# Optimization experiments

Hardware: AMD Instinct MI355X
Metric: run time of the kernel (lower is better)

The kernel has to match this reference:

```python
import jax, jax.numpy as jnp
import numpy as np

RADIUS = 0.1
NSAMPLE = 32


def _ball_query(new_xyz, xyz, radius, nsample):
    # new_xyz: (B, S, 3), xyz: (B, N, 3) -> idx (B, S, nsample) int32
    N = xyz.shape[1]
    d2 = jnp.sum((new_xyz[:, :, None, :] - xyz[:, None, :, :]) ** 2, axis=-1)  # (B,S,N)
    mask = d2 < radius * radius
    cand = jnp.where(mask, jnp.arange(N, dtype=jnp.int32)[None, None, :], N)
    cand = jnp.sort(cand, axis=-1)[:, :, :nsample]  # first nsample in-ball indices
    first = cand[:, :, :1]
    first = jnp.where(first == N, 0, first)  # empty ball -> index 0 (CUDA semantics)
    return jnp.where(cand == N, first, cand).astype(jnp.int32)


def _group(features, idx):
    # features: (B, C, N), idx: (B, S, K) -> (B, C, S, K)
    return jax.vmap(lambda f, i: f[:, i])(features, idx)


def setup_inputs() -> dict:
    key = jax.random.key(0)
    k1, k2, k3, k4 = jax.random.split(key, 4)
    B, N, S, C = 4, 16384, 2048, 64
    xyz = jax.random.uniform(k1, (B, N, 3), dtype=jnp.float32)
    new_xyz = jax.random.uniform(k2, (B, S, 3), dtype=jnp.float32)
    features = jax.random.normal(k3, (B, C, N), dtype=jnp.float32)
    fps_idx = jax.random.randint(k4, (B, S), 0, N, dtype=jnp.int32)
    return {"xyz": xyz, "new_xyz": new_xyz, "features": features, "fps_idx": fps_idx}


def reference(xyz, new_xyz, features, fps_idx):
    idx = _ball_query(new_xyz, xyz, RADIUS, NSAMPLE)          # (B,S,nsample)
    idx = jnp.concatenate([fps_idx[:, :, None], idx], axis=2)  # (B,S,nsample+1)
    xyz_t = jnp.transpose(xyz, (0, 2, 1))                      # (B,3,N)
    raw_grouped_xyz = _group(xyz_t, idx)                       # (B,3,S,K)
    grouped_xyz = raw_grouped_xyz - jnp.transpose(new_xyz, (0, 2, 1))[..., None]
    grouped_features = _group(features, idx)                   # (B,C,S,K)
    return jnp.concatenate([raw_grouped_xyz, grouped_xyz, grouped_features], axis=1)
```

## Files before the change

### kernel.cpp

```cpp
#include <hip/hip_runtime.h>

#define BB 4
#define NN 16384
#define SS 2048
#define CC 64
#define NS 32
#define KK 33
#define OC 70
#define SCH 4
#define GT 512
#define NC 10
#define NCELL 1000
#define CCAP 64
#define HCAP 224
#define RPAD 0.100001f

__device__ __forceinline__ float sq_nofma(float v) {
  float r = v * v;
  asm volatile("" : "+v"(r));
  return r;
}

__device__ __forceinline__ int cell1(float x) {
  int c = (int)(x * 10.0f);
  return c < 0 ? 0 : (c > 9 ? 9 : c);
}
__device__ __forceinline__ int cell3(float x, float y, float z) {
  return (cell1(z) * NC + cell1(y)) * NC + cell1(x);
}

__device__ __forceinline__ void ball_query_wave(
    const float* __restrict__ xb, float qx, float qy, float qz, int lane,
    int* out) {
  const float R2 = 0.01f;
  int cnt = 0;
  int firstIdx = 0;
  for (int base = 0; base < NN; base += 256) {
    float px[4], py[4], pz[4];
#pragma unroll
    for (int j = 0; j < 4; ++j) {
      int n = base + j * 64 + lane;
      const float* p = xb + n * 3;
      px[j] = p[0]; py[j] = p[1]; pz[j] = p[2];
    }
#pragma unroll
    for (int j = 0; j < 4; ++j) {
      float dx = px[j] - qx, dy = py[j] - qy, dz = pz[j] - qz;
      float d2 = sq_nofma(dx) + sq_nofma(dy);
      asm volatile("" : "+v"(d2));
      d2 = d2 + sq_nofma(dz);
      bool m = d2 < R2;
      unsigned long long bal = __ballot(m);
      if (cnt == 0 && bal) firstIdx = base + j * 64 + __builtin_ctzll(bal);
      int pos = cnt + (int)__popcll(bal & ((1ull << lane) - 1ull));
      if (m && pos < NS) out[pos] = base + j * 64 + lane;
      cnt += (int)__popcll(bal);
    }
    if (cnt >= NS) break;
  }
  if (cnt < NS) {
    int pad = (cnt == 0) ? 0 : firstIdx;
    if (lane >= cnt && lane < NS) out[lane] = pad;
  }
}

__global__ __launch_bounds__(256) void qg_tr_build(
    const float* __restrict__ xyz, const float* __restrict__ feat,
    float* __restrict__ featT, int* __restrict__ cnt, int* __restrict__ ovf,
    float4* __restrict__ ptsc) {
  __shared__ float tile[32 * 260];
  const int bid = (int)blockIdx.x;
  const int tid = (int)threadIdx.x;
  const int b = bid >> 7;
  const int rest = bid & 127;
  const int n0 = (rest >> 1) << 8;
  const int cc = rest & 1;
  const int c0 = cc << 5;
  const int wv = tid >> 6, lane = tid & 63;

  if (cc == 0) {
    const int n = n0 + tid;
    const float* p = xyz + ((size_t)b * NN + n) * 3;
    float x = p[0], y = p[1], z = p[2];
    int cell = cell3(x, y, z);
    int pos = atomicAdd(&cnt[(b << 10) + cell], 1);
    if (pos < CCAP) {
      ptsc[((((size_t)b << 10) + cell) << 6) + pos] =
          make_float4(x, y, z, __int_as_float(n));
    } else {
      atomicOr(&ovf[b], 1);
    }
  }

  const float* fb = feat + ((size_t)b * CC + c0) * NN + n0;
#pragma unroll
  for (int rr = 0; rr < 8; ++rr) {
    int c = rr * 4 + wv;
    float4 v = *(const float4*)(fb + (size_t)c * NN + 4 * lane);
    *(float4*)&tile[c * 260 + 4 * lane] = v;
  }
  __syncthreads();
  const int c4 = lane & 7, m = lane >> 3;
  float4* oT = (float4*)(featT + ((size_t)b * NN + n0) * CC);
#pragma unroll
  for (int it = 0; it < 8; ++it) {
    int n = it * 32 + wv * 8 + m;
    float4 v;
    v.x = tile[(4 * c4 + 0) * 260 + n];
    v.y = tile[(4 * c4 + 1) * 260 + n];
    v.z = tile[(4 * c4 + 2) * 260 + n];
    v.w = tile[(4 * c4 + 3) * 260 + n];
    oT[(size_t)n * (CC / 4) + (c0 >> 2) + c4] = v;
  }
}

__global__ __launch_bounds__(GT) void qg_main(
    const float* __restrict__ xyz, const float* __restrict__ nxyz,
    const float4* __restrict__ ptsc, const int* __restrict__ cnt,
    const int* __restrict__ ovf, const float* __restrict__ featT,
    const int* __restrict__ fps, float* __restrict__ out) {
  __shared__ float sf[CC][SCH * KK + 1];
  __shared__ int sidx[SCH * KK];
  __shared__ int hitbuf[SCH][HCAP];
  const int tid = (int)threadIdx.x;
  const int blk = (int)blockIdx.x;
  const int b = blk >> 9;
  const int s0 = (blk & 511) * SCH;
  const int wv = tid >> 6, lane = tid & 63;

  if (wv < SCH) {
    const int q = b * SS + s0 + wv;
    const float R2 = 0.01f;
    float qx = nxyz[q * 3 + 0];
    float qy = nxyz[q * 3 + 1];
    float qz = nxyz[q * 3 + 2];
    int* hb = hitbuf[wv];
    int* qout = &sidx[wv * KK];

    if (ovf[b]) {
      ball_query_wave(xyz + (size_t)b * NN * 3, qx, qy, qz, lane, qout + 1);
    } else {
      int lox = max(0, (int)floorf((qx - RPAD) * 10.f));
      int hix = min(9, (int)floorf((qx + RPAD) * 10.f));
      int loy = max(0, (int)floorf((qy - RPAD) * 10.f));
      int hiy = min(9, (int)floorf((qy + RPAD) * 10.f));
      int loz = max(0, (int)floorf((qz - RPAD) * 10.f));
      int hiz = min(9, (int)floorf((qz + RPAD) * 10.f));
      const int ncx = hix - lox + 1, ncy = hiy - loy + 1, ncz = hiz - loz + 1;
      const int ncell = ncx * ncy * ncz;

      const int* cntb = cnt + (b << 10);
      int cell_l = 0, cnt_l = 0;
      if (lane < ncell) {
        int iz = lane / (ncx * ncy);
        int r = lane - iz * ncx * ncy;
        int iy = r / ncx, ix = r - iy * ncx;
        cell_l = ((loz + iz) * NC + (loy + iy)) * NC + (lox + ix);
        cnt_l = cntb[cell_l];
      }

      const float4* pcb = ptsc + ((size_t)b << 16);
      const unsigned long long lt = (1ull << lane) - 1ull;
      const int slot = lane & 31;
      const int half = lane >> 5;
      int hcnt = 0;
      const int npair = (ncell + 1) >> 1;

      int c0 = __shfl(cell_l, 0, 64);
      int c1 = __shfl(cell_l, 1, 64);
      float4 vnext = pcb[(((half ? c1 : c0)) << 6) + slot];

      for (int p = 0; p < npair; ++p) {
        float4 v = vnext;
        int m0 = __shfl(cnt_l, 2 * p, 64);
        int m1 = __shfl(cnt_l, 2 * p + 1, 64);
        int cme0 = __shfl(cell_l, 2 * p, 64);
        int cme1 = __shfl(cell_l, 2 * p + 1, 64);
        if (p + 1 < npair) {
          int n0 = __shfl(cell_l, 2 * p + 2, 64);
          int n1 = __shfl(cell_l, 2 * p + 3, 64);
          vnext = pcb[(((half ? n1 : n0)) << 6) + slot];
        }
        int m = half ? m1 : m0;
        {
          float dx = v.x - qx, dy = v.y - qy, dz = v.z - qz;
          float d2 = sq_nofma(dx) + sq_nofma(dy);
          asm volatile("" : "+v"(d2));
          d2 = d2 + sq_nofma(dz);
          bool hit = (slot < m) && (d2 < R2);
          unsigned long long bal = __ballot(hit);
          if (hit) {
            int pos = hcnt + (int)__popcll(bal & lt);
            if (pos < HCAP) hb[pos] = __float_as_int(v.w);
          }
          hcnt += (int)__popcll(bal);
        }
        if (m0 > 32 || m1 > 32) {
          float4 w = pcb[(((half ? cme1 : cme0)) << 6) + 32 + slot];
          float dx = w.x - qx, dy = w.y - qy, dz = w.z - qz;
          float d2 = sq_nofma(dx) + sq_nofma(dy);
          asm volatile("" : "+v"(d2));
          d2 = d2 + sq_nofma(dz);
          bool hit = (32 + slot < m) && (d2 < R2);
          unsigned long long bal = __ballot(hit);
          if (hit) {
            int pos = hcnt + (int)__popcll(bal & lt);
            if (pos < HCAP) hb[pos] = __float_as_int(w.w);
          }
          hcnt += (int)__popcll(bal);
        }
      }

      asm volatile("s_waitcnt lgkmcnt(0)" ::: "memory");
      const int M = hcnt;
      if (M > HCAP) {
        ball_query_wave(xyz + (size_t)b * NN * 3, qx, qy, qz, lane, qout + 1);
      } else {
        int minv = 0x7fffffff;
        for (int i = lane; i < M; i += 64) {
          int hh = hb[i];
          minv = min(minv, hh);
          int rank = 0;
          for (int j = 0; j < M; ++j) rank += (hb[j] < hh) ? 1 : 0;
          if (rank < NS) qout[1 + rank] = hh;
        }
        if (M < NS) {
#pragma unroll
          for (int d = 1; d < 64; d <<= 1)
            minv = min(minv, __shfl_xor(minv, d, 64));
          int pad = (M == 0) ? 0 : minv;
          if (lane >= M && lane < NS) qout[1 + lane] = pad;
        }
      }
    }
    if (lane == 0) qout[0] = fps[q];
  }
  __syncthreads();

  const size_t cstr = (size_t)SS * KK;
  const float4* fT4 = (const float4*)(featT + (size_t)b * NN * CC);
  int e = tid & 15;
  for (int pp = tid >> 4; pp < SCH * KK; pp += GT / 16) {
    int n = sidx[pp];
    float4 v = fT4[(size_t)n * (CC / 4) + e];
    sf[4 * e + 0][pp] = v.x;
    sf[4 * e + 1][pp] = v.y;
    sf[4 * e + 2][pp] = v.z;
    sf[4 * e + 3][pp] = v.w;
  }

  if (tid < SCH * KK) {
    int s4 = tid / KK;
    int n = sidx[tid];
    const float* p = xyz + ((size_t)b * NN + n) * 3;
    float x = p[0], y = p[1], z = p[2];
    int q = b * SS + s0 + s4;
    float cx = nxyz[q * 3 + 0], cy = nxyz[q * 3 + 1], cz = nxyz[q * 3 + 2];
    size_t obase = ((size_t)(b * OC) * SS + s0) * KK + tid;
    out[obase + 0 * cstr] = x;
    out[obase + 1 * cstr] = y;
    out[obase + 2 * cstr] = z;
    out[obase + 3 * cstr] = x - cx;
    out[obase + 4 * cstr] = y - cy;
    out[obase + 5 * cstr] = z - cz;
  }
  __syncthreads();

  size_t fbase = ((size_t)(b * OC + 6) * SS + s0) * KK;
  for (int idx = tid; idx < CC * SCH * KK; idx += GT) {
    int c = idx / (SCH * KK);
    int j = idx - c * (SCH * KK);
    out[fbase + (size_t)c * cstr + j] = sf[c][j];
  }
}

__global__ __launch_bounds__(256) void qg_ballq(
    const float* __restrict__ xyz, const float* __restrict__ nxyz,
    int* __restrict__ wsidx) {
  int q = (int)((blockIdx.x * blockDim.x + threadIdx.x) >> 6);
  int lane = (int)(threadIdx.x & 63);
  int b = q / SS;
  const float* xb = xyz + (size_t)b * NN * 3;
  ball_query_wave(xb, nxyz[q * 3], nxyz[q * 3 + 1], nxyz[q * 3 + 2], lane,
                  wsidx + (size_t)q * NS);
}

__global__ __launch_bounds__(256) void qg_gather(
    const float* __restrict__ xyz, const float* __restrict__ nxyz,
    const float* __restrict__ feat, const int* __restrict__ fps,
    const int* __restrict__ wsidx, float* __restrict__ out) {
  unsigned t = blockIdx.x * 256u + threadIdx.x;
  const unsigned TOT = (unsigned)BB * OC * SS * KK;
  if (t >= TOT) return;
  unsigned k = t % KK;
  unsigned r = t / KK;
  unsigned s = r % SS;
  r /= SS;
  unsigned c = r % OC;
  unsigned b = r / OC;
  unsigned q = b * SS + s;
  int n = (k == 0) ? fps[q] : wsidx[(size_t)q * NS + (k - 1)];
  float v;
  if (c < 6) {
    unsigned cc = (c < 3) ? c : c - 3;
    v = xyz[((size_t)b * NN + (unsigned)n) * 3 + cc];
    if (c >= 3) v -= nxyz[q * 3 + cc];
  } else {
    v = feat[((size_t)b * CC + (c - 6)) * NN + (unsigned)n];
  }
  out[t] = v;
}

__global__ __launch_bounds__(256) void qg_fused(
    const float* __restrict__ xyz, const float* __restrict__ nxyz,
    const float* __restrict__ feat, const int* __restrict__ fps,
    float* __restrict__ out) {
  __shared__ int sidx[4][KK];
  int wv = (int)(threadIdx.x >> 6), lane = (int)(threadIdx.x & 63);
  int q = (int)blockIdx.x * 4 + wv;
  int b = q / SS, s = q % SS;
  const float* xb = xyz + (size_t)b * NN * 3;
  ball_query_wave(xb, nxyz[q * 3], nxyz[q * 3 + 1], nxyz[q * 3 + 2], lane,
                  &sidx[wv][1]);
  if (lane == 0) sidx[wv][0] = fps[q];
  __syncthreads();
  for (int f = lane; f < OC * KK; f += 64) {
    int c = f / KK, k = f - c * KK;
    int n = sidx[wv][k];
    float v;
    if (c < 6) {
      int cc = (c < 3) ? c : c - 3;
      v = xb[n * 3 + cc];
      if (c >= 3) v -= nxyz[q * 3 + cc];
    } else {
      v = feat[((size_t)b * CC + (c - 6)) * NN + n];
    }
    out[((size_t)((size_t)b * OC + c) * SS + s) * KK + k] = v;
  }
}

extern "C" void kernel_launch(void* const* d_in, const int* in_sizes, int n_in,
                              void* d_out, int out_size, void* d_ws, size_t ws_size,
                              hipStream_t stream) {
  const float* xyz  = (const float*)d_in[0];
  const float* nxyz = (const float*)d_in[1];
  const float* feat = (const float*)d_in[2];
  const int*   fps  = (const int*)d_in[3];
  float* out = (float*)d_out;

  const size_t ptsc_b  = (size_t)BB * 1024 * CCAP * sizeof(float4);
  const size_t cnt_b   = 32768;
  const size_t featT_b = (size_t)BB * NN * CC * sizeof(float);
  const size_t grid_need = ptsc_b + cnt_b + featT_b;

  const size_t idx_b = (size_t)BB * SS * NS * sizeof(int);

  if (ws_size >= grid_need) {
    char* w = (char*)d_ws;
    float4* ptsc  = (float4*)w;                      w += ptsc_b;
    int*    cnt   = (int*)w;                         w += cnt_b;
    float*  featT = (float*)w;
    int*    ovf   = cnt + BB * 1024;
    hipMemsetAsync(cnt, 0, cnt_b, stream);
    qg_tr_build<<<512, 256, 0, stream>>>(xyz, feat, featT, cnt, ovf, ptsc);
    qg_main<<<BB * (SS / SCH), GT, 0, stream>>>(xyz, nxyz, ptsc, cnt, ovf,
                                                featT, fps, out);
  } else if (ws_size >= idx_b) {
    int* wsidx = (int*)d_ws;
    qg_ballq<<<(BB * SS) / 4, 256, 0, stream>>>(xyz, nxyz, wsidx);
    unsigned tot = (unsigned)BB * OC * SS * KK;
    qg_gather<<<(tot + 255u) / 256u, 256, 0, stream>>>(xyz, nxyz, feat, fps,
                                                       wsidx, out);
  } else {
    qg_fused<<<(BB * SS) / 4, 256, 0, stream>>>(xyz, nxyz, feat, fps, out);
  }
}
```

Baseline: 53.81 us.

## Split ball-query cell scan across two waves per query and batch feature gathers

```diff
diff --git a/kernel.cpp b/kernel.cpp
--- a/kernel.cpp
+++ b/kernel.cpp
@@ -13,6 +13,7 @@
 #define NCELL 1000
 #define CCAP 64
 #define HCAP 224
+#define HSEG 112
 #define RPAD 0.100001f
 
 __device__ __forceinline__ float sq_nofma(float v) {
@@ -122,100 +123,117 @@
   __shared__ float sf[CC][SCH * KK + 1];
   __shared__ int sidx[SCH * KK];
   __shared__ int hitbuf[SCH][HCAP];
+  __shared__ int hcnt_s[SCH][2];
   const int tid = (int)threadIdx.x;
   const int blk = (int)blockIdx.x;
   const int b = blk >> 9;
   const int s0 = (blk & 511) * SCH;
   const int wv = tid >> 6, lane = tid & 63;
-
-  if (wv < SCH) {
-    const int q = b * SS + s0 + wv;
-    const float R2 = 0.01f;
-    float qx = nxyz[q * 3 + 0];
-    float qy = nxyz[q * 3 + 1];
-    float qz = nxyz[q * 3 + 2];
-    int* hb = hitbuf[wv];
-    int* qout = &sidx[wv * KK];
-
-    if (ovf[b]) {
+  const int wq = wv >> 1;
+  const int h = wv & 1;
+  const int q = b * SS + s0 + wq;
+  const float R2 = 0.01f;
+  const float qx = nxyz[q * 3 + 0];
+  const float qy = nxyz[q * 3 + 1];
+  const float qz = nxyz[q * 3 + 2];
+  int* hb = hitbuf[wq];
+  int* qout = &sidx[wq * KK];
+  const bool bad = ovf[b] != 0;
+
+  if (!bad) {
+    int lox = max(0, (int)floorf((qx - RPAD) * 10.f));
+    int hix = min(9, (int)floorf((qx + RPAD) * 10.f));
+    int loy = max(0, (int)floorf((qy - RPAD) * 10.f));
+    int hiy = min(9, (int)floorf((qy + RPAD) * 10.f));
+    int loz = max(0, (int)floorf((qz - RPAD) * 10.f));
+    int hiz = min(9, (int)floorf((qz + RPAD) * 10.f));
+    const int ncx = hix - lox + 1, ncy = hiy - loy + 1, ncz = hiz - loz + 1;
+    const int ncell = ncx * ncy * ncz;
+
+    const int* cntb = cnt + (b << 10);
+    int cell_l = 0, cnt_l = 0;
+    if (lane < ncell) {
+      int iz = lane / (ncx * ncy);
+      int r = lane - iz * ncx * ncy;
+      int iy = r / ncx, ix = r - iy * ncx;
+      cell_l = ((loz + iz) * NC + (loy + iy)) * NC + (lox + ix);
+      cnt_l = cntb[cell_l];
+    }
+
+    const float4* pcb = ptsc + ((size_t)b << 16);
+    const unsigned long long lt = (1ull << lane) - 1ull;
+    const int slot = lane & 31;
+    const int half = lane >> 5;
+    const int npair = (ncell + 1) >> 1;
+    const int hp2 = (npair + 1) >> 1;
+    const int p_beg = h * hp2;
+    const int p_end = min(npair, p_beg + hp2);
+    const int wbase = h * HSEG;
+    int hcnt = 0;
+
+#define PAIRLOAD(pp)                                                       \
+  ({                                                                       \
+    int pc_ = ((pp) < p_end) ? (pp) : p_beg;                               \
+    int ca_ = __shfl(cell_l, 2 * pc_, 64);                                 \
+    int cb_ = __shfl(cell_l, 2 * pc_ + 1, 64);                             \
+    pcb[(((half ? cb_ : ca_)) << 6) + slot];                               \
+  })
+
+    float4 v0 = PAIRLOAD(p_beg);
+    float4 v1 = PAIRLOAD(p_beg + 1);
+    for (int p = p_beg; p < p_end; ++p) {
+      float4 v = v0;
+      v0 = v1;
+      v1 = PAIRLOAD(p + 2);
+      int m0 = __shfl(cnt_l, 2 * p, 64);
+      int m1 = __shfl(cnt_l, 2 * p + 1, 64);
+      int m = half ? m1 : m0;
+      {
+        float dx = v.x - qx, dy = v.y - qy, dz = v.z - qz;
+        float d2 = sq_nofma(dx) + sq_nofma(dy);
+        asm volatile("" : "+v"(d2));
+        d2 = d2 + sq_nofma(dz);
+        bool hit = (slot < m) && (d2 < R2);
+        unsigned long long bal = __ballot(hit);
+        if (hit) {
+          int pos = hcnt + (int)__popcll(bal & lt);
+          if (pos < HSEG) hb[wbase + pos] = __float_as_int(v.w);
+        }
+        hcnt += (int)__popcll(bal);
+      }
+      if (m0 > 32 || m1 > 32) {
+        int ca = __shfl(cell_l, 2 * p, 64);
+        int cb = __shfl(cell_l, 2 * p + 1, 64);
+        float4 w = pcb[(((half ? cb : ca)) << 6) + 32 + slot];
+        float dx = w.x - qx, dy = w.y - qy, dz = w.z - qz;
+        float d2 = sq_nofma(dx) + sq_nofma(dy);
+        asm volatile("" : "+v"(d2));
+        d2 = d2 + sq_nofma(dz);
+        bool hit = (32 + slot < m) && (d2 < R2);
+        unsigned long long bal = __ballot(hit);
+        if (hit) {
+          int pos = hcnt + (int)__popcll(bal & lt);
+          if (pos < HSEG) hb[wbase + pos] = __float_as_int(w.w);
+        }
+        hcnt += (int)__popcll(bal);
+      }
+    }
+#undef PAIRLOAD
+    if (lane == 0) hcnt_s[wq][h] = hcnt;
+  }
+  __syncthreads();
+
+  if (h == 0) {
+    if (bad) {
       ball_query_wave(xyz + (size_t)b * NN * 3, qx, qy, qz, lane, qout + 1);
     } else {
-      int lox = max(0, (int)floorf((qx - RPAD) * 10.f));
-      int hix = min(9, (int)floorf((qx + RPAD) * 10.f));
-      int loy = max(0, (int)floorf((qy - RPAD) * 10.f));
-      int hiy = min(9, (int)floorf((qy + RPAD) * 10.f));
-      int loz = max(0, (int)floorf((qz - RPAD) * 10.f));
-      int hiz = min(9, (int)floorf((qz + RPAD) * 10.f));
-      const int ncx = hix - lox + 1, ncy = hiy - loy + 1, ncz = hiz - loz + 1;
-      const int ncell = ncx * ncy * ncz;
-
-      const int* cntb = cnt + (b << 10);
-      int cell_l = 0, cnt_l = 0;
-      if (lane < ncell) {
-        int iz = lane / (ncx * ncy);
-        int r = lane - iz * ncx * ncy;
-        int iy = r / ncx, ix = r - iy * ncx;
-        cell_l = ((loz + iz) * NC + (loy + iy)) * NC + (lox + ix);
-        cnt_l = cntb[cell_l];
-      }
-
-      const float4* pcb = ptsc + ((size_t)b << 16);
-      const unsigned long long lt = (1ull << lane) - 1ull;
-      const int slot = lane & 31;
-      const int half = lane >> 5;
-      int hcnt = 0;
-      const int npair = (ncell + 1) >> 1;
-
-      int c0 = __shfl(cell_l, 0, 64);
-      int c1 = __shfl(cell_l, 1, 64);
-      float4 vnext = pcb[(((half ? c1 : c0)) << 6) + slot];
-
-      for (int p = 0; p < npair; ++p) {
-        float4 v = vnext;
-        int m0 = __shfl(cnt_l, 2 * p, 64);
-        int m1 = __shfl(cnt_l, 2 * p + 1, 64);
-        int cme0 = __shfl(cell_l, 2 * p, 64);
-        int cme1 = __shfl(cell_l, 2 * p + 1, 64);
-        if (p + 1 < npair) {
-          int n0 = __shfl(cell_l, 2 * p + 2, 64);
-          int n1 = __shfl(cell_l, 2 * p + 3, 64);
-          vnext = pcb[(((half ? n1 : n0)) << 6) + slot];
-        }
-        int m = half ? m1 : m0;
-        {
-          float dx = v.x - qx, dy = v.y - qy, dz = v.z - qz;
-          float d2 = sq_nofma(dx) + sq_nofma(dy);
-          asm volatile("" : "+v"(d2));
-          d2 = d2 + sq_nofma(dz);
-          bool hit = (slot < m) && (d2 < R2);
-          unsigned long long bal = __ballot(hit);
-          if (hit) {
-            int pos = hcnt + (int)__popcll(bal & lt);
-            if (pos < HCAP) hb[pos] = __float_as_int(v.w);
-          }
-          hcnt += (int)__popcll(bal);
-        }
-        if (m0 > 32 || m1 > 32) {
-          float4 w = pcb[(((half ? cme1 : cme0)) << 6) + 32 + slot];
-          float dx = w.x - qx, dy = w.y - qy, dz = w.z - qz;
-          float d2 = sq_nofma(dx) + sq_nofma(dy);
-          asm volatile("" : "+v"(d2));
-          d2 = d2 + sq_nofma(dz);
-          bool hit = (32 + slot < m) && (d2 < R2);
-          unsigned long long bal = __ballot(hit);
-          if (hit) {
-            int pos = hcnt + (int)__popcll(bal & lt);
-            if (pos < HCAP) hb[pos] = __float_as_int(w.w);
-          }
-          hcnt += (int)__popcll(bal);
-        }
-      }
-
-      asm volatile("s_waitcnt lgkmcnt(0)" ::: "memory");
-      const int M = hcnt;
-      if (M > HCAP) {
+      const int MA = hcnt_s[wq][0], MB = hcnt_s[wq][1];
+      if (MA > HSEG || MB > HSEG) {
         ball_query_wave(xyz + (size_t)b * NN * 3, qx, qy, qz, lane, qout + 1);
       } else {
+        for (int t = lane; t < MB; t += 64) hb[MA + t] = hb[HSEG + t];
+        asm volatile("s_waitcnt lgkmcnt(0)" ::: "memory");
+        const int M = MA + MB;
         int minv = 0x7fffffff;
         for (int i = lane; i < M; i += 64) {
           int hh = hb[i];
@@ -239,14 +257,43 @@
 
   const size_t cstr = (size_t)SS * KK;
   const float4* fT4 = (const float4*)(featT + (size_t)b * NN * CC);
-  int e = tid & 15;
-  for (int pp = tid >> 4; pp < SCH * KK; pp += GT / 16) {
-    int n = sidx[pp];
-    float4 v = fT4[(size_t)n * (CC / 4) + e];
-    sf[4 * e + 0][pp] = v.x;
-    sf[4 * e + 1][pp] = v.y;
-    sf[4 * e + 2][pp] = v.z;
-    sf[4 * e + 3][pp] = v.w;
+  {
+    const int e = tid & 15;
+    const int g = tid >> 4;
+    const bool has4 = (g + 128) < SCH * KK;
+    int n0_ = sidx[g];
+    int n1_ = sidx[g + 32];
+    int n2_ = sidx[g + 64];
+    int n3_ = sidx[g + 96];
+    int n4_ = has4 ? sidx[g + 128] : 0;
+    float4 w0 = fT4[(size_t)n0_ * (CC / 4) + e];
+    float4 w1 = fT4[(size_t)n1_ * (CC / 4) + e];
+    float4 w2 = fT4[(size_t)n2_ * (CC / 4) + e];
+    float4 w3 = fT4[(size_t)n3_ * (CC / 4) + e];
+    float4 w4 = has4 ? fT4[(size_t)n4_ * (CC / 4) + e]
+                     : make_float4(0.f, 0.f, 0.f, 0.f);
+    sf[4 * e + 0][g] = w0.x;
+    sf[4 * e + 1][g] = w0.y;
+    sf[4 * e + 2][g] = w0.z;
+    sf[4 * e + 3][g] = w0.w;
+    sf[4 * e + 0][g + 32] = w1.x;
+    sf[4 * e + 1][g + 32] = w1.y;
+    sf[4 * e + 2][g + 32] = w1.z;
+    sf[4 * e + 3][g + 32] = w1.w;
+    sf[4 * e + 0][g + 64] = w2.x;
+    sf[4 * e + 1][g + 64] = w2.y;
+    sf[4 * e + 2][g + 64] = w2.z;
+    sf[4 * e + 3][g + 64] = w2.w;
+    sf[4 * e + 0][g + 96] = w3.x;
+    sf[4 * e + 1][g + 96] = w3.y;
+    sf[4 * e + 2][g + 96] = w3.z;
+    sf[4 * e + 3][g + 96] = w3.w;
+    if (has4) {
+      sf[4 * e + 0][g + 128] = w4.x;
+      sf[4 * e + 1][g + 128] = w4.y;
+      sf[4 * e + 2][g + 128] = w4.z;
+      sf[4 * e + 3][g + 128] = w4.w;
+    }
   }
 
   if (tid < SCH * KK) {
@@ -254,8 +301,8 @@
     int n = sidx[tid];
     const float* p = xyz + ((size_t)b * NN + n) * 3;
     float x = p[0], y = p[1], z = p[2];
-    int q = b * SS + s0 + s4;
-    float cx = nxyz[q * 3 + 0], cy = nxyz[q * 3 + 1], cz = nxyz[q * 3 + 2];
+    int qq = b * SS + s0 + s4;
+    float cx = nxyz[qq * 3 + 0], cy = nxyz[qq * 3 + 1], cz = nxyz[qq * 3 + 2];
     size_t obase = ((size_t)(b * OC) * SS + s0) * KK + tid;
     out[obase + 0 * cstr] = x;
     out[obase + 1 * cstr] = y;
```

Result: faster. 51.88 us (-3.6%).
